# Kernel optimization log

Hardware: AMD Instinct MI355X
Metric: run time of the kernel (lower is better)

## Reference

```python
import jax, jax.numpy as jnp
import numpy as np

K = 40  # knn_graph(pos, 40, loop=False)


def _knn_idx(pos):
    # pos: [N,3] -> [N,K] indices of K nearest neighbors (self excluded)
    d2 = jnp.sum((pos[:, None, :] - pos[None, :, :]) ** 2, axis=-1)  # [N,N]
    n = pos.shape[0]
    d2 = jnp.where(jnp.eye(n, dtype=bool), jnp.inf, d2)  # loop=False
    _, idx = jax.lax.top_k(-d2, K)
    return idx


def setup_inputs() -> dict:
    key = jax.random.key(0)
    ks = jax.random.split(key, 4)
    B, N, F, H, O = 8, 4096, 8, 64, 128
    x = jax.random.normal(ks[0], (B, N, F), dtype=jnp.float32)
    pos = jax.random.normal(ks[1], (B, N, 3), dtype=jnp.float32)
    W1 = jax.random.normal(ks[2], (F + 3, H), dtype=jnp.float32) / np.sqrt(F + 3)
    b1 = jnp.zeros((H,), dtype=jnp.float32)
    W2 = jax.random.normal(ks[3], (H, O), dtype=jnp.float32) / np.sqrt(H)
    b2 = jnp.zeros((O,), dtype=jnp.float32)
    return {"x": x, "pos": pos, "W1": W1, "b1": b1, "W2": W2, "b2": b2}


def reference(x, pos, W1, b1, W2, b2):
    B, N, F = x.shape
    idx = jax.vmap(_knn_idx)(pos)  # [B,N,K] source indices per target node
    # PyG PointConv add_self_loops=True: append a self edge per node
    self_idx = jnp.broadcast_to(jnp.arange(N)[None, :, None], (B, N, 1))
    idx_sl = jnp.concatenate([idx, self_idx], axis=-1)  # [B,N,K+1]
    gather = jax.vmap(lambda a, i: a[i])  # per-cloud gather
    x_j = gather(x, idx_sl)                       # [B,N,K+1,F]
    rel = gather(pos, idx_sl) - pos[:, :, None, :]  # [B,N,K+1,3] pos_j - pos_i
    # local_nn: Linear -> ReLU -> Linear on concat([x_j, rel])
    msg_in = jnp.concatenate([x_j, rel], axis=-1)  # [B,N,K+1,F+3]
    h = jax.nn.relu(jnp.einsum('bnkf,fh->bnkh', msg_in, W1) + b1)
    m = jnp.einsum('bnkh,ho->bnko', h, W2) + b2   # [B,N,K+1,O]
    out = jnp.max(m, axis=2)                       # max aggregation -> [B,N,O]
    # reconstruct edge_index with global node ids (matches knn_graph output set)
    offs = (jnp.arange(B) * N)[:, None, None]
    src = (idx + offs).reshape(-1)
    tgt = jnp.broadcast_to(jnp.arange(N)[None, :, None] + offs, (B, N, K)).reshape(-1)
    edge_index = jnp.stack([src, tgt])  # [2, B*N*K], flow source_to_target
    return out, edge_index
```

## Files before the change

### kernel.cpp

```cpp
#include <hip/hip_runtime.h>
#include <stdint.h>

#define N_NODES 4096
#define K_NN    40
#define B_CLOUDS 8
#define F_IN    8
#define H_DIM   64
#define O_DIM   128

#define OUT_FEAT_ELEMS (B_CLOUDS * N_NODES * O_DIM)
#define EDGES          (B_CLOUDS * N_NODES * K_NN)

typedef short bf16x8 __attribute__((ext_vector_type(8)));
typedef float f32x4  __attribute__((ext_vector_type(4)));

__device__ __forceinline__ unsigned short f2bf(float f) {
    unsigned u = __float_as_uint(f);
    unsigned r = (u + 0x7FFFu + ((u >> 16) & 1u)) >> 16;
    return (unsigned short)r;
}

__device__ __forceinline__ unsigned shr1_dpp(unsigned v) {
    return (unsigned)__builtin_amdgcn_update_dpp(0, (int)v, 0x138, 0xF, 0xF, true);
}

#define INS_STEP(mask_, dreg_, Rhi_, Rlo_)                                         \
    {                                                                              \
        const int src = (int)__builtin_ctzll(mask_);                               \
        mask_ &= mask_ - 1;                                                        \
        const unsigned long long kb =                                              \
            ((unsigned long long)(unsigned)__builtin_amdgcn_readlane((int)(dreg_), src) << 32) \
            | (unsigned)((c << 6) | src);                                          \
        const unsigned long long RP = ((unsigned long long)Rhi_ << 32) | Rlo_;     \
        const bool keep = (RP <= kb);                                              \
        const unsigned uplo = shr1_dpp(Rlo_);                                      \
        const unsigned uphi = shr1_dpp(Rhi_);                                      \
        const unsigned long long up = ((unsigned long long)uphi << 32) | uplo;     \
        const unsigned long long mx = (up > kb) ? up : kb;                         \
        const unsigned long long nw = keep ? RP : mx;                              \
        Rhi_ = (unsigned)(nw >> 32);                                               \
        Rlo_ = (unsigned)nw;                                                       \
    }

__global__ __launch_bounds__(1024, 8) void knn_kernel(const float* __restrict__ pos,
                                                      float* __restrict__ out)
{
    __shared__ float4 ppos[N_NODES];
    __shared__ unsigned long long qual[16][2][64];

    const int b  = blockIdx.x >> 7;
    const int i0 = (blockIdx.x & 127) << 5;
    const float* posb = pos + (size_t)b * N_NODES * 3;

    for (int n = threadIdx.x; n < N_NODES; n += 1024) {
        ppos[n] = make_float4(posb[3 * n], posb[3 * n + 1], posb[3 * n + 2], 0.f);
    }
    __syncthreads();

    const int wave = threadIdx.x >> 6;
    const int lane = threadIdx.x & 63;
    const int iA = i0 + (wave << 1);
    const int iB = iA + 1;

    const float4 pa4 = ppos[iA];
    const float4 pb4 = ppos[iB];
    const float pax = pa4.x, pay = pa4.y, paz = pa4.z;
    const float pbx = pb4.x, pby = pb4.y, pbz = pb4.z;

    unsigned mA0 = ~0u, mA1 = ~0u, mA2 = ~0u, mA3 = ~0u;
    unsigned mB0 = ~0u, mB1 = ~0u, mB2 = ~0u, mB3 = ~0u;
#pragma unroll 8
    for (int c = 0; c < 64; ++c) {
        const float4 p = ppos[(c << 6) | lane];
        const float dxA = __fsub_rn(pax, p.x);
        const float dyA = __fsub_rn(pay, p.y);
        const float dzA = __fsub_rn(paz, p.z);
        const float d2A = __fadd_rn(__fadd_rn(__fmul_rn(dxA, dxA), __fmul_rn(dyA, dyA)),
                                    __fmul_rn(dzA, dzA));
        const float dxB = __fsub_rn(pbx, p.x);
        const float dyB = __fsub_rn(pby, p.y);
        const float dzB = __fsub_rn(pbz, p.z);
        const float d2B = __fadd_rn(__fadd_rn(__fmul_rn(dxB, dxB), __fmul_rn(dyB, dyB)),
                                    __fmul_rn(dzB, dzB));
        const unsigned dA = __float_as_uint(d2A);
        const unsigned dB = __float_as_uint(d2B);
        if ((c & 3) == 0)      { mA0 = min(mA0, dA); mB0 = min(mB0, dB); }
        else if ((c & 3) == 1) { mA1 = min(mA1, dA); mB1 = min(mB1, dB); }
        else if ((c & 3) == 2) { mA2 = min(mA2, dA); mB2 = min(mB2, dB); }
        else                   { mA3 = min(mA3, dA); mB3 = min(mB3, dB); }
    }

    unsigned accA = 0, accB = 0;
    for (int bit = 30; bit >= 13; --bit) {
        const unsigned tA = accA | (1u << bit);
        const unsigned tB = accB | (1u << bit);
        const int cA = __popcll(__ballot(mA0 < tA)) + __popcll(__ballot(mA1 < tA))
                     + __popcll(__ballot(mA2 < tA)) + __popcll(__ballot(mA3 < tA));
        const int cB = __popcll(__ballot(mB0 < tB)) + __popcll(__ballot(mB1 < tB))
                     + __popcll(__ballot(mB2 < tB)) + __popcll(__ballot(mB3 < tB));
        if (cA <= K_NN) accA = tA;
        if (cB <= K_NN) accB = tB;
    }
    const unsigned thA = accA | 0x1FFFu;
    const unsigned thB = accB | 0x1FFFu;

    unsigned long long* qA = qual[wave][0];
    unsigned long long* qB = qual[wave][1];
    int baseA = 0, baseB = 0;
#pragma unroll 4
    for (int c = 0; c < 64; ++c) {
        const float4 p = ppos[(c << 6) | lane];
        const float dxA = __fsub_rn(pax, p.x);
        const float dyA = __fsub_rn(pay, p.y);
        const float dzA = __fsub_rn(paz, p.z);
        const float d2A = __fadd_rn(__fadd_rn(__fmul_rn(dxA, dxA), __fmul_rn(dyA, dyA)),
                                    __fmul_rn(dzA, dzA));
        const float dxB = __fsub_rn(pbx, p.x);
        const float dyB = __fsub_rn(pby, p.y);
        const float dzB = __fsub_rn(pbz, p.z);
        const float d2B = __fadd_rn(__fadd_rn(__fmul_rn(dxB, dxB), __fmul_rn(dyB, dyB)),
                                    __fmul_rn(dzB, dzB));
        const unsigned dA = __float_as_uint(d2A);
        const unsigned dB = __float_as_uint(d2B);
        const unsigned jj = (unsigned)((c << 6) | lane);

        const bool sA = dA <= thA;
        const unsigned long long mkA = __ballot(sA);
        const unsigned mbA = __builtin_amdgcn_mbcnt_hi(
            (unsigned)(mkA >> 32), __builtin_amdgcn_mbcnt_lo((unsigned)mkA, 0u));
        const int idxA = baseA + (int)mbA;
        if (sA && idxA < 64)
            qA[idxA] = ((unsigned long long)dA << 32) | jj;
        baseA += (int)__popcll(mkA);

        const bool sB = dB <= thB;
        const unsigned long long mkB = __ballot(sB);
        const unsigned mbB = __builtin_amdgcn_mbcnt_hi(
            (unsigned)(mkB >> 32), __builtin_amdgcn_mbcnt_lo((unsigned)mkB, 0u));
        const int idxB = baseB + (int)mbB;
        if (sB && idxB < 64)
            qB[idxB] = ((unsigned long long)dB << 32) | jj;
        baseB += (int)__popcll(mkB);
    }

    float* src_out = out + OUT_FEAT_ELEMS;
    float* tgt_out = src_out + EDGES;
    const int giA = b * N_NODES + iA;
    const int giB = giA + 1;

    if (baseA <= 64 && baseB <= 64) {
        unsigned long long keyA = (lane < baseA) ? qA[lane] : ~0ull;
        unsigned long long keyB = (lane < baseB) ? qB[lane] : ~0ull;
#pragma unroll
        for (int k = 2; k <= 64; k <<= 1) {
#pragma unroll
            for (int j = k >> 1; j > 0; j >>= 1) {
                const unsigned long long prtA = __shfl_xor(keyA, j, 64);
                const unsigned long long prtB = __shfl_xor(keyB, j, 64);
                const bool up = (lane & k) == 0;
                const bool takeMin = (((lane & j) == 0) == up);
                const bool lessA = keyA < prtA;
                const unsigned long long mnA = lessA ? keyA : prtA;
                const unsigned long long mxA = lessA ? prtA : keyA;
                keyA = takeMin ? mnA : mxA;
                const bool lessB = keyB < prtB;
                const unsigned long long mnB = lessB ? keyB : prtB;
                const unsigned long long mxB = lessB ? prtB : keyB;
                keyB = takeMin ? mnB : mxB;
            }
        }
        const unsigned loA = (unsigned)keyA;
        const unsigned loB = (unsigned)keyB;
        const int psA = (int)__builtin_ctzll(__ballot(loA == (unsigned)iA));
        const int psB = (int)__builtin_ctzll(__ballot(loB == (unsigned)iB));
        const int elA = lane - (lane > psA ? 1 : 0);
        const int elB = lane - (lane > psB ? 1 : 0);
        if (lane != psA && elA < K_NN) {
            src_out[(size_t)giA * K_NN + elA] = (float)(b * N_NODES + (int)loA);
            tgt_out[(size_t)giA * K_NN + elA] = (float)giA;
        }
        if (lane != psB && elB < K_NN) {
            src_out[(size_t)giB * K_NN + elB] = (float)(b * N_NODES + (int)loB);
            tgt_out[(size_t)giB * K_NN + elB] = (float)giB;
        }
    } else {
        const int ci = iA >> 6;
        const int liA = iA & 63;
        const int liB = iB & 63;
        unsigned RAhi = (lane == 0) ? 0u : 0xFFFFFFFFu;
        unsigned RAlo = (lane == 0) ? 0u : 0xFFFFFFFFu;
        unsigned RBhi = RAhi, RBlo = RAlo;
        for (int c = 0; c < 64; ++c) {
            const float4 p = ppos[(c << 6) | lane];
            const float dxA = __fsub_rn(pax, p.x);
            const float dyA = __fsub_rn(pay, p.y);
            const float dzA = __fsub_rn(paz, p.z);
            const float d2A = __fadd_rn(__fadd_rn(__fmul_rn(dxA, dxA), __fmul_rn(dyA, dyA)),
                                        __fmul_rn(dzA, dzA));
            const float dxB = __fsub_rn(pbx, p.x);
            const float dyB = __fsub_rn(pby, p.y);
            const float dzB = __fsub_rn(pbz, p.z);
            const float d2B = __fadd_rn(__fadd_rn(__fmul_rn(dxB, dxB), __fmul_rn(dyB, dyB)),
                                        __fmul_rn(dzB, dzB));
            const unsigned dA = __float_as_uint(d2A);
            const unsigned dB = __float_as_uint(d2B);
            unsigned long long maskA = __ballot(dA <= thA);
            unsigned long long maskB = __ballot(dB <= thB);
            if (c == ci) {
                maskA &= ~(1ull << liA);
                maskB &= ~(1ull << liB);
            }
            while (maskA) INS_STEP(maskA, dA, RAhi, RAlo);
            while (maskB) INS_STEP(maskB, dB, RBhi, RBlo);
        }
        const unsigned el = (unsigned)(lane - 1);
        if (el < K_NN) {
            src_out[(size_t)giA * K_NN + el] = (float)(b * N_NODES + (int)RAlo);
            tgt_out[(size_t)giA * K_NN + el] = (float)giA;
            src_out[(size_t)giB * K_NN + el] = (float)(b * N_NODES + (int)RBlo);
            tgt_out[(size_t)giB * K_NN + el] = (float)giB;
        }
    }
}

__global__ __launch_bounds__(256) void prep_kernel(const float* __restrict__ W2,
                                                   const float* __restrict__ W1,
                                                   unsigned short* __restrict__ ws)
{
    const int idx = blockIdx.x * 256 + threadIdx.x;
    if (idx < 8192) {
        const int j    = idx & 7;
        const int lane = (idx >> 3) & 63;
        const int kt   = (idx >> 9) & 1;
        const int nt   = idx >> 10;
        const int k = kt * 32 + (lane >> 4) * 8 + j;
        const int n = nt * 16 + (lane & 15);
        ws[idx] = f2bf(W2[k * O_DIM + n]);
    } else if (idx < 8192 + 2048) {
        const int t = idx - 8192;
        const int j    = t & 7;
        const int lane = (t >> 3) & 63;
        const int nt   = t >> 9;
        const int k = (lane >> 4) * 8 + j;
        const int n = nt * 16 + (lane & 15);
        ws[idx] = (k < 11) ? f2bf(W1[k * H_DIM + n]) : (unsigned short)0;
    }
}

#define HSTR 72
#define KSTR 40

__global__ __launch_bounds__(256, 4) void conv_kernel(
    const float* __restrict__ x, const float* __restrict__ pos,
    const unsigned short* __restrict__ w2f,
    const unsigned short* __restrict__ w1f,
    const float* __restrict__ b1, const float* __restrict__ b2,
    float* __restrict__ out)
{
    __shared__ __align__(16) unsigned short Hh[4][48 * HSTR];

    const int b    = blockIdx.x >> 10;
    const int i0   = (blockIdx.x & 1023) << 2;
    const int wave = threadIdx.x >> 6;
    const int lane = threadIdx.x & 63;
    const int quad = lane >> 4;
    const int col  = lane & 15;
    const int i    = i0 + wave;
    const int gi   = b * N_NODES + i;

    unsigned short* Hw = Hh[wave];

    const float* src_edges = out + OUT_FEAT_ELEMS;
    if (lane < 48) {
        int j;
        if (lane < K_NN) j = (int)src_edges[(size_t)gi * K_NN + lane] - b * N_NODES;
        else             j = i;
        const float* xr = x + ((size_t)b * N_NODES + j) * F_IN;
        float4 xa = *(const float4*)xr;
        float4 xb = *(const float4*)(xr + 4);
        const float* pj = pos + ((size_t)b * N_NODES + j) * 3;
        const float* pi = pos + ((size_t)b * N_NODES + i) * 3;
        unsigned w[16];
#pragma unroll
        for (int t = 0; t < 16; ++t) w[t] = 0;
        w[0] = (unsigned)f2bf(xa.x) | ((unsigned)f2bf(xa.y) << 16);
        w[1] = (unsigned)f2bf(xa.z) | ((unsigned)f2bf(xa.w) << 16);
        w[2] = (unsigned)f2bf(xb.x) | ((unsigned)f2bf(xb.y) << 16);
        w[3] = (unsigned)f2bf(xb.z) | ((unsigned)f2bf(xb.w) << 16);
        w[4] = (unsigned)f2bf(pj[0] - pi[0]) | ((unsigned)f2bf(pj[1] - pi[1]) << 16);
        w[5] = (unsigned)f2bf(pj[2] - pi[2]);
        unsigned* mrow = (unsigned*)(Hw + lane * KSTR);
        *(uint4*)(mrow)      = make_uint4(w[0], w[1], w[2], w[3]);
        *(uint4*)(mrow + 4)  = make_uint4(w[4], w[5], w[6], w[7]);
        *(uint4*)(mrow + 8)  = make_uint4(w[8], w[9], w[10], w[11]);
        *(uint4*)(mrow + 12) = make_uint4(w[12], w[13], w[14], w[15]);
    }

    bf16x8 Am[3];
#pragma unroll
    for (int mt = 0; mt < 3; ++mt)
        Am[mt] = *(const bf16x8*)&Hw[(mt * 16 + col) * KSTR + quad * 8];

    const bf16x8* W1f = (const bf16x8*)w1f;
    float hreg[12][4];
#pragma unroll
    for (int nt = 0; nt < 4; ++nt) {
        bf16x8 Bn = W1f[nt * 64 + lane];
        const float bias = b1[nt * 16 + col];
        f32x4 d0 = {bias, bias, bias, bias};
        f32x4 d1 = d0, d2 = d0;
        d0 = __builtin_amdgcn_mfma_f32_16x16x32_bf16(Am[0], Bn, d0, 0, 0, 0);
        d1 = __builtin_amdgcn_mfma_f32_16x16x32_bf16(Am[1], Bn, d1, 0, 0, 0);
        d2 = __builtin_amdgcn_mfma_f32_16x16x32_bf16(Am[2], Bn, d2, 0, 0, 0);
#pragma unroll
        for (int r = 0; r < 4; ++r) {
            hreg[nt * 3 + 0][r] = fmaxf(d0[r], 0.0f);
            hreg[nt * 3 + 1][r] = fmaxf(d1[r], 0.0f);
            hreg[nt * 3 + 2][r] = fmaxf(d2[r], 0.0f);
        }
    }

#pragma unroll
    for (int nt = 0; nt < 4; ++nt)
#pragma unroll
        for (int mt = 0; mt < 3; ++mt)
#pragma unroll
            for (int r = 0; r < 4; ++r)
                Hw[(mt * 16 + quad * 4 + r) * HSTR + nt * 16 + col] =
                    f2bf(hreg[nt * 3 + mt][r]);

    bf16x8 Af[3][2];
#pragma unroll
    for (int mt = 0; mt < 3; ++mt)
#pragma unroll
        for (int kt = 0; kt < 2; ++kt)
            Af[mt][kt] = *(const bf16x8*)&Hw[(mt * 16 + col) * HSTR + kt * 32 + quad * 8];

    const bf16x8* Bws = (const bf16x8*)w2f;
#pragma unroll
    for (int nt = 0; nt < 8; ++nt) {
        bf16x8 B0 = Bws[nt * 128 + lane];
        bf16x8 B1 = Bws[nt * 128 + 64 + lane];

        f32x4 c0 = {0.f, 0.f, 0.f, 0.f};
        f32x4 c1 = {0.f, 0.f, 0.f, 0.f};
        f32x4 c2 = {0.f, 0.f, 0.f, 0.f};
        c0 = __builtin_amdgcn_mfma_f32_16x16x32_bf16(Af[0][0], B0, c0, 0, 0, 0);
        c1 = __builtin_amdgcn_mfma_f32_16x16x32_bf16(Af[1][0], B0, c1, 0, 0, 0);
        c2 = __builtin_amdgcn_mfma_f32_16x16x32_bf16(Af[2][0], B0, c2, 0, 0, 0);
        c0 = __builtin_amdgcn_mfma_f32_16x16x32_bf16(Af[0][1], B1, c0, 0, 0, 0);
        c1 = __builtin_amdgcn_mfma_f32_16x16x32_bf16(Af[1][1], B1, c1, 0, 0, 0);
        c2 = __builtin_amdgcn_mfma_f32_16x16x32_bf16(Af[2][1], B1, c2, 0, 0, 0);

        float vm = c0[0];
        vm = fmaxf(vm, c0[1]); vm = fmaxf(vm, c0[2]); vm = fmaxf(vm, c0[3]);
        vm = fmaxf(vm, c1[0]); vm = fmaxf(vm, c1[1]); vm = fmaxf(vm, c1[2]); vm = fmaxf(vm, c1[3]);
        vm = fmaxf(vm, c2[0]); vm = fmaxf(vm, c2[1]); vm = fmaxf(vm, c2[2]); vm = fmaxf(vm, c2[3]);
        vm = fmaxf(vm, __shfl_xor(vm, 16));
        vm = fmaxf(vm, __shfl_xor(vm, 32));
        vm += b2[nt * 16 + col];

        if (lane < 16) out[(size_t)gi * O_DIM + nt * 16 + lane] = vm;
    }
}

extern "C" void kernel_launch(void* const* d_in, const int* in_sizes, int n_in,
                              void* d_out, int out_size, void* d_ws, size_t ws_size,
                              hipStream_t stream) {
    const float* x   = (const float*)d_in[0];
    const float* pos = (const float*)d_in[1];
    const float* W1  = (const float*)d_in[2];
    const float* b1  = (const float*)d_in[3];
    const float* W2  = (const float*)d_in[4];
    const float* b2  = (const float*)d_in[5];
    float* out = (float*)d_out;
    unsigned short* ws = (unsigned short*)d_ws;

    prep_kernel<<<40, 256, 0, stream>>>(W2, W1, ws);
    knn_kernel<<<(B_CLOUDS * N_NODES) / 32, 1024, 0, stream>>>(pos, out);
    conv_kernel<<<(B_CLOUDS * N_NODES) / 4, 256, 0, stream>>>(
        x, pos, ws, ws + 8192, b1, b2, out);
}
```

Before: 196.4 us.

## Skip candidate-free chunks in KNN selection pass and use DPP/swizzle bitonic sort

The first distance pass now gives each lane its own contiguous block of 64 points, using an XOR-swizzled index to avoid LDS bank conflicts. Each lane's minimum distance then says whether its block can hold any candidate below the threshold. The second pass walks only the flagged blocks through a ballot mask, instead of all 64, cutting repeated distance work and LDS traffic. The bitonic sort of candidates swaps generic 64-bit shuffles for DPP quad permutes, ds_swizzle, and one shuffle, to lower cross-lane exchange cost. The data-dependent while loop adds scalar control overhead and brings little saving when candidates spread across most blocks.

New measurement: 188.8 us. 3.9% less time.

```diff
diff --git a/kernel.cpp b/kernel.cpp
--- a/kernel.cpp
+++ b/kernel.cpp
@@ -42,6 +42,33 @@
         Rlo_ = (unsigned)nw;                                                       \
     }
 
+#define DPPX1(v)  ((unsigned)__builtin_amdgcn_update_dpp(0, (int)(v), 0xB1, 0xF, 0xF, true))
+#define DPPX2(v)  ((unsigned)__builtin_amdgcn_update_dpp(0, (int)(v), 0x4E, 0xF, 0xF, true))
+#define SWZ4(v)   ((unsigned)__builtin_amdgcn_ds_swizzle((int)(v), 0x101F))
+#define SWZ8(v)   ((unsigned)__builtin_amdgcn_ds_swizzle((int)(v), 0x201F))
+#define SWZ16(v)  ((unsigned)__builtin_amdgcn_ds_swizzle((int)(v), 0x401F))
+#define SX32(v)   ((unsigned)__shfl_xor((int)(v), 32, 64))
+
+#define CE(K, J, SH)                                                         \
+    {                                                                        \
+        const unsigned pAl = SH((unsigned)keyA);                             \
+        const unsigned pAh = SH((unsigned)(keyA >> 32));                     \
+        const unsigned pBl = SH((unsigned)keyB);                             \
+        const unsigned pBh = SH((unsigned)(keyB >> 32));                     \
+        const unsigned long long pA = ((unsigned long long)pAh << 32) | pAl; \
+        const unsigned long long pB = ((unsigned long long)pBh << 32) | pBl; \
+        const bool up = (lane & (K)) == 0;                                   \
+        const bool tk = ((lane & (J)) == 0) == up;                           \
+        const bool lA = keyA < pA;                                           \
+        const unsigned long long mnA = lA ? keyA : pA;                       \
+        const unsigned long long mxA = lA ? pA : keyA;                       \
+        keyA = tk ? mnA : mxA;                                               \
+        const bool lB = keyB < pB;                                           \
+        const unsigned long long mnB = lB ? keyB : pB;                       \
+        const unsigned long long mxB = lB ? pB : keyB;                       \
+        keyB = tk ? mnB : mxB;                                               \
+    }
+
 __global__ __launch_bounds__(1024, 8) void knn_kernel(const float* __restrict__ pos,
                                                       float* __restrict__ out)
 {
@@ -71,7 +98,8 @@
     unsigned mB0 = ~0u, mB1 = ~0u, mB2 = ~0u, mB3 = ~0u;
 #pragma unroll 8
     for (int c = 0; c < 64; ++c) {
-        const float4 p = ppos[(c << 6) | lane];
+        const int jj = (lane << 6) | (c ^ lane);
+        const float4 p = ppos[jj];
         const float dxA = __fsub_rn(pax, p.x);
         const float dyA = __fsub_rn(pay, p.y);
         const float dzA = __fsub_rn(paz, p.z);
@@ -104,11 +132,16 @@
     const unsigned thA = accA | 0x1FFFu;
     const unsigned thB = accB | 0x1FFFu;
 
+    const unsigned bmA = min(min(mA0, mA1), min(mA2, mA3));
+    const unsigned bmB = min(min(mB0, mB1), min(mB2, mB3));
+    unsigned long long sm = __ballot(bmA <= thA) | __ballot(bmB <= thB);
+
     unsigned long long* qA = qual[wave][0];
     unsigned long long* qB = qual[wave][1];
     int baseA = 0, baseB = 0;
-#pragma unroll 4
-    for (int c = 0; c < 64; ++c) {
+    while (sm) {
+        const int c = (int)__builtin_ctzll(sm);
+        sm &= sm - 1;
         const float4 p = ppos[(c << 6) | lane];
         const float dxA = __fsub_rn(pax, p.x);
         const float dyA = __fsub_rn(pay, p.y);
@@ -151,24 +184,12 @@
     if (baseA <= 64 && baseB <= 64) {
         unsigned long long keyA = (lane < baseA) ? qA[lane] : ~0ull;
         unsigned long long keyB = (lane < baseB) ? qB[lane] : ~0ull;
-#pragma unroll
-        for (int k = 2; k <= 64; k <<= 1) {
-#pragma unroll
-            for (int j = k >> 1; j > 0; j >>= 1) {
-                const unsigned long long prtA = __shfl_xor(keyA, j, 64);
-                const unsigned long long prtB = __shfl_xor(keyB, j, 64);
-                const bool up = (lane & k) == 0;
-                const bool takeMin = (((lane & j) == 0) == up);
-                const bool lessA = keyA < prtA;
-                const unsigned long long mnA = lessA ? keyA : prtA;
-                const unsigned long long mxA = lessA ? prtA : keyA;
-                keyA = takeMin ? mnA : mxA;
-                const bool lessB = keyB < prtB;
-                const unsigned long long mnB = lessB ? keyB : prtB;
-                const unsigned long long mxB = lessB ? prtB : keyB;
-                keyB = takeMin ? mnB : mxB;
-            }
-        }
+        CE(2, 1, DPPX1)
+        CE(4, 2, DPPX2)  CE(4, 1, DPPX1)
+        CE(8, 4, SWZ4)   CE(8, 2, DPPX2)  CE(8, 1, DPPX1)
+        CE(16, 8, SWZ8)  CE(16, 4, SWZ4)  CE(16, 2, DPPX2) CE(16, 1, DPPX1)
+        CE(32, 16, SWZ16) CE(32, 8, SWZ8) CE(32, 4, SWZ4)  CE(32, 2, DPPX2) CE(32, 1, DPPX1)
+        CE(64, 32, SX32) CE(64, 16, SWZ16) CE(64, 8, SWZ8) CE(64, 4, SWZ4)  CE(64, 2, DPPX2) CE(64, 1, DPPX1)
         const unsigned loA = (unsigned)keyA;
         const unsigned loB = (unsigned)keyB;
         const int psA = (int)__builtin_ctzll(__ballot(loA == (unsigned)iA));
```
